# Optimization experiments

Measured on AMD Instinct MI355X. Metric: run time of the kernel, lower is better.

Reference implementation:

```python
import jax, jax.numpy as jnp
import numpy as np

B, N, D = 4, 300, 256
G, PIN, POUT = 4, 32, 128
CG = D // G
TOTAL = CG * CG + PIN * POUT
STRIDES = (8, 16, 32, 64)
SIZES = ((100, 160), (50, 80), (25, 40), (13, 20))
TAU = 2.0
MAP_STRIDE = 3.0  # log2(stride of level 0) = log2(8)


def setup_inputs():
    key = jax.random.key(0)
    ks = jax.random.split(key, 16)
    inp = {}
    for i, (h, w) in enumerate(SIZES):
        inp['feat%d' % i] = jax.random.normal(ks[i], (B, D, h, w), jnp.float32)
    inp['query_feat'] = jax.random.normal(ks[4], (B, N, D), jnp.float32)
    xy = jax.random.uniform(ks[5], (B, N, 2), jnp.float32) * jnp.array([1280.0, 800.0], jnp.float32)
    z = jax.random.uniform(ks[6], (B, N, 1), jnp.float32) * 2.0 + 4.0
    r = jax.random.normal(ks[7], (B, N, 1), jnp.float32) * 0.3
    inp['query_roi'] = jnp.concatenate([xy, z, r], axis=-1)
    inp['off_w'] = jax.random.normal(ks[8], (D, G * PIN * 3), jnp.float32) * 0.01
    bias = jnp.concatenate([jax.random.uniform(ks[9], (G, PIN, 2), jnp.float32, -0.5, 0.5),
                            jnp.full((G, PIN, 1), -1.0, jnp.float32)], axis=-1)
    inp['off_b'] = bias.reshape(-1)
    inp['pg_w'] = jax.random.normal(ks[10], (D, G * TOTAL), jnp.float32) * 0.02
    inp['pg_b'] = jnp.zeros((G * TOTAL,), jnp.float32)
    inp['op_w'] = jax.random.normal(ks[11], (G * POUT * CG, D), jnp.float32) * 0.01
    inp['op_b'] = jnp.zeros((D,), jnp.float32)
    inp['ln_g'] = jnp.ones((D,), jnp.float32)
    inp['ln_b'] = jnp.zeros((D,), jnp.float32)
    return inp


def _ln2(x, eps=1e-5):
    # F.layer_norm over last two dims, no affine
    mu = jnp.mean(x, axis=(-2, -1), keepdims=True)
    var = jnp.mean((x - mu) ** 2, axis=(-2, -1), keepdims=True)
    return (x - mu) * jax.lax.rsqrt(var + eps)


def _ln1(x, eps=1e-5):
    mu = jnp.mean(x, axis=-1, keepdims=True)
    var = jnp.mean((x - mu) ** 2, axis=-1, keepdims=True)
    return (x - mu) * jax.lax.rsqrt(var + eps)


def _bilinear(feat, px, py, w):
    # feat [B,D,H,W]; px,py,w [B,N,G,PIN] (pixel coords, grid_sample align_corners=False, zero pad)
    H, W = feat.shape[2], feat.shape[3]
    v = feat.reshape(B, G, CG, H * W).transpose(0, 1, 3, 2)  # [B,G,HW,CG]
    x0 = jnp.floor(px)
    y0 = jnp.floor(py)
    wx1 = px - x0
    wy1 = py - y0

    def corner(xf, yf, cw):
        xi = xf.astype(jnp.int32)
        yi = yf.astype(jnp.int32)
        valid = (xi >= 0) & (xi < W) & (yi >= 0) & (yi < H)
        idx = jnp.clip(yi, 0, H - 1) * W + jnp.clip(xi, 0, W - 1)       # [B,N,G,PIN]
        idx = idx.transpose(0, 2, 1, 3).reshape(B, G, N * PIN, 1)
        g = jnp.take_along_axis(v, idx, axis=2)                          # [B,G,N*PIN,CG]
        g = g.reshape(B, G, N, PIN, CG).transpose(0, 2, 1, 3, 4)
        return g * (cw * valid.astype(cw.dtype))[..., None]

    acc = (corner(x0, y0, (1 - wx1) * (1 - wy1)) + corner(x0 + 1, y0, wx1 * (1 - wy1)) +
           corner(x0, y0 + 1, (1 - wx1) * wy1) + corner(x0 + 1, y0 + 1, wx1 * wy1))
    return acc * w[..., None]


def _forward(feats, query_feat, query_roi, off_w, off_b, pg_w, pg_b, op_w, op_b, ln_g, ln_b):
    # make_sample_points
    offset = (query_feat @ off_w + off_b).reshape(B, N, G * PIN, 3)
    roi_cc = query_roi[..., :2]
    scale = 2.0 ** query_roi[..., 2:3]
    ratio = 2.0 ** jnp.concatenate([query_roi[..., 3:4] * -0.5, query_roi[..., 3:4] * 0.5], axis=-1)
    roi_wh = scale * ratio                                               # [B,N,2]
    sample_xy = roi_cc[:, :, None, :] + offset[..., :2] * roi_wh[:, :, None, :]  # [B,N,G*PIN,2]
    sample_z = query_roi[..., 2:3] + offset[..., 2]                      # [B,N,G*PIN]
    # level weights: softmax over levels of -(z-3-l)^2/tau
    lvl = jnp.arange(len(STRIDES), dtype=sample_z.dtype)
    lw = jax.nn.softmax(-((sample_z - MAP_STRIDE)[..., None] - lvl) ** 2 / TAU, axis=-1)
    sx = sample_xy[..., 0].reshape(B, N, G, PIN)
    sy = sample_xy[..., 1].reshape(B, N, G, PIN)
    sampled = jnp.zeros((B, N, G, PIN, CG), query_feat.dtype)
    for li, (feat, stride) in enumerate(zip(feats, STRIDES)):
        wl = lw[..., li].reshape(B, N, G, PIN)
        sampled = sampled + _bilinear(feat, sx / stride - 0.5, sy / stride - 0.5, wl)
    # AdaptiveMixing
    params = (query_feat @ pg_w + pg_b).reshape(B, N, G, TOTAL)
    M = params[..., :CG * CG].reshape(B, N, G, CG, CG)
    S = params[..., CG * CG:].reshape(B, N, G, POUT, PIN)
    h = jnp.einsum('bngpc,bngcd->bngpd', sampled, M)
    h = jax.nn.relu(_ln2(h))
    h = jnp.einsum('bngop,bngpd->bngod', S, h)
    h = jax.nn.relu(_ln2(h))
    h = query_feat + (h.reshape(B, N, G * POUT * CG) @ op_w + op_b)
    return _ln1(h) * ln_g + ln_b


def reference(feat0, feat1, feat2, feat3, query_feat, query_roi, off_w, off_b, pg_w, pg_b, op_w, op_b, ln_g, ln_b):
    return _forward([feat0, feat1, feat2, feat3], query_feat, query_roi,
                    off_w, off_b, pg_w, pg_b, op_w, op_b, ln_g, ln_b)
```

## Files before the change

### kernel.cpp

```cpp
#include <hip/hip_runtime.h>
#include <hip/hip_bf16.h>
#include <cstdint>

namespace {

constexpr int B = 4, N = 300, D = 256;
constexpr int G = 4, PIN = 32, POUT = 128;
constexpr int CG = D / G;
constexpr int TOTAL = CG * CG + PIN * POUT;
constexpr int BN_TOT = B * N;
constexpr int BN_PAD = 1216;
constexpr int GT = G * TOTAL;

typedef short s16x8 __attribute__((ext_vector_type(8)));
typedef float f32x4 __attribute__((ext_vector_type(4)));

__device__ __forceinline__ float bf2f(unsigned short u) {
  union { unsigned int i; float f; } x; x.i = ((unsigned int)u) << 16; return x.f;
}
__device__ __forceinline__ unsigned short f2bf(float f) {
  union { float f; unsigned int i; } x; x.f = f;
  unsigned int r = x.i + 0x7fffu + ((x.i >> 16) & 1u);
  return (unsigned short)(r >> 16);
}

__device__ __forceinline__ void breduce2(float& a, float& b, volatile float* red) {
  __syncthreads();
  #pragma unroll
  for (int off = 32; off; off >>= 1) {
    a += __shfl_down(a, off, 64);
    b += __shfl_down(b, off, 64);
  }
  int t = threadIdx.x;
  if ((t & 63) == 0) { red[t >> 6] = a; red[4 + (t >> 6)] = b; }
  __syncthreads();
  a = red[0] + red[1] + red[2] + red[3];
  b = red[4] + red[5] + red[6] + red[7];
}

__global__ __launch_bounds__(256) void k_transpose(
    const float* __restrict__ in, unsigned short* __restrict__ out, int R, int C,
    int mperm) {
  __shared__ unsigned short T[64][72];
  int c0 = blockIdx.x * 64;
  int r0 = blockIdx.y * 64;
  int t = threadIdx.x;
  #pragma unroll
  for (int i = 0; i < 4; ++i) {
    int u = t + i * 256;
    int rr = u >> 4, c4 = (u & 15) * 4;
    float4 v = *(const float4*)(in + (size_t)(r0 + rr) * C + c0 + c4);
    ushort4 w;
    w.x = f2bf(v.x); w.y = f2bf(v.y); w.z = f2bf(v.z); w.w = f2bf(v.w);
    *(ushort4*)&T[rr][c4] = w;
  }
  __syncthreads();
  #pragma unroll
  for (int i = 0; i < 2; ++i) {
    int u = t + i * 256;
    int c = u >> 3, rr8 = (u & 7) * 8;
    unsigned short tmp[8];
    #pragma unroll
    for (int j = 0; j < 8; ++j) tmp[j] = T[rr8 + j][c];
    int n = c0 + c;
    if (mperm) {
      int local = n & 8191;
      if (local < 4096) n = (n & ~8191) | ((local & 63) << 6) | (local >> 6);
    }
    *(uint4*)(out + (size_t)n * R + r0 + rr8) = *(const uint4*)tmp;
  }
}

__global__ __launch_bounds__(256) void k_featT(
    const float* __restrict__ in, unsigned short* __restrict__ out, int HW) {
  __shared__ unsigned short T[64][72];
  int hw0 = blockIdx.x * 64;
  int d0 = blockIdx.y * 64;
  int bb = blockIdx.z;
  int t = threadIdx.x;
  #pragma unroll
  for (int i = 0; i < 4; ++i) {
    int u = t + i * 256;
    int rr = u >> 4, c4 = (u & 15) * 4;
    if (hw0 + c4 + 3 < HW) {
      float4 v = *(const float4*)(in + ((size_t)(bb * D + d0 + rr)) * HW + hw0 + c4);
      ushort4 w;
      w.x = f2bf(v.x); w.y = f2bf(v.y); w.z = f2bf(v.z); w.w = f2bf(v.w);
      *(ushort4*)&T[rr][c4] = w;
    }
  }
  __syncthreads();
  #pragma unroll
  for (int i = 0; i < 2; ++i) {
    int u = t + i * 256;
    int p = u >> 3, dd8 = (u & 7) * 8;
    if (hw0 + p < HW) {
      unsigned short tmp[8];
      #pragma unroll
      for (int j = 0; j < 8; ++j) tmp[j] = T[dd8 + j][p];
      *(uint4*)(out + ((size_t)(bb * HW + hw0 + p)) * D + d0 + dd8) = *(const uint4*)tmp;
    }
  }
}

__global__ __launch_bounds__(256) void k_cvt_qf(
    const float* __restrict__ qf, unsigned short* __restrict__ qb) {
  int e = (blockIdx.x * 256 + threadIdx.x) * 4;
  int row = e >> 8;
  ushort4 w;
  if (row < BN_TOT) {
    float4 v = *(const float4*)(qf + e);
    w.x = f2bf(v.x); w.y = f2bf(v.y); w.z = f2bf(v.z); w.w = f2bf(v.w);
  } else {
    w.x = w.y = w.z = w.w = 0;
  }
  *(ushort4*)(qb + e) = w;
}

__global__ __launch_bounds__(384) void k_off(
    const float* __restrict__ qf, const float* __restrict__ offw,
    const float* __restrict__ offb, float* __restrict__ offsets) {
  int r0 = blockIdx.x * 16;
  int t = threadIdx.x;
  __shared__ float Q[16][256];
  for (int i = t; i < 16 * 256; i += 384)
    Q[i >> 8][i & 255] = qf[(size_t)(r0 + (i >> 8)) * 256 + (i & 255)];
  __syncthreads();
  float acc[16];
  float bias = offb[t];
  #pragma unroll
  for (int r = 0; r < 16; ++r) acc[r] = bias;
  for (int d = 0; d < 256; ++d) {
    float w = offw[(size_t)d * 384 + t];
    #pragma unroll
    for (int r = 0; r < 16; ++r) acc[r] += Q[r][d] * w;
  }
  #pragma unroll
  for (int r = 0; r < 16; ++r) offsets[(size_t)(r0 + r) * 384 + t] = acc[r];
}

__global__ __launch_bounds__(256) void k_gather(
    const float* __restrict__ roi, const float* __restrict__ offsets,
    const unsigned short* __restrict__ featT, unsigned short* __restrict__ sampled) {
  int bn = blockIdx.x;
  int bb = bn / N;
  int t = threadIdx.x;
  __shared__ int   widx[2048];
  __shared__ float wval[2048];

  const int Wl[4] = {160, 80, 40, 20};
  const int Hl[4] = {100, 50, 25, 13};
  const int loff[4] = {0, 16384000, 20480000, 21504000};
  const int HWl[4] = {16000, 4000, 1000, 260};
  const float sl[4] = {8.f, 16.f, 32.f, 64.f};

  float cx = roi[bn * 4 + 0], cy = roi[bn * 4 + 1];
  float z = roi[bn * 4 + 2], r = roi[bn * 4 + 3];
  float scale = exp2f(z);
  float rwx = scale * exp2f(-0.5f * r);
  float rhy = scale * exp2f(0.5f * r);

  #pragma unroll
  for (int task = t; task < 512; task += 256) {
    int j = task >> 2, l = task & 3;
    float ox = offsets[(size_t)bn * 384 + j * 3 + 0];
    float oy = offsets[(size_t)bn * 384 + j * 3 + 1];
    float oz = offsets[(size_t)bn * 384 + j * 3 + 2];
    float sx = cx + ox * rwx;
    float sy = cy + oy * rhy;
    float sz = z + oz;
    float lw[4];
    float m = -1e30f;
    #pragma unroll
    for (int ll = 0; ll < 4; ++ll) {
      float dlt = sz - 3.0f - (float)ll;
      lw[ll] = -dlt * dlt * 0.5f;
      m = fmaxf(m, lw[ll]);
    }
    float s = 0.f;
    #pragma unroll
    for (int ll = 0; ll < 4; ++ll) { lw[ll] = expf(lw[ll] - m); s += lw[ll]; }
    float wl_ = lw[l] / s;

    int W = Wl[l], H = Hl[l];
    float px = sx / sl[l] - 0.5f;
    float py = sy / sl[l] - 0.5f;
    float x0f = floorf(px), y0f = floorf(py);
    int x0 = (int)x0f, y0 = (int)y0f;
    float fx = px - x0f, fy = py - y0f;
    int base = loff[l] + bb * HWl[l] * 256;
    #pragma unroll
    for (int k = 0; k < 4; ++k) {
      int xi = x0 + (k & 1), yi = y0 + (k >> 1);
      bool valid = (xi >= 0) & (xi < W) & (yi >= 0) & (yi < H);
      int xc = min(max(xi, 0), W - 1), yc = min(max(yi, 0), H - 1);
      float wgt = ((k & 1) ? fx : 1.f - fx) * ((k >> 1) ? fy : 1.f - fy) * wl_;
      widx[j * 16 + l * 4 + k] = base + (yc * W + xc) * 256;
      wval[j * 16 + l * 4 + k] = valid ? wgt : 0.f;
    }
  }
  __syncthreads();

  int wave = t >> 6, lane = t & 63;
  int half = lane >> 5, ln = lane & 31;
  const unsigned short* fb = featT + wave * 64 + ln * 2;
  #pragma unroll 2
  for (int it = 0; it < 16; ++it) {
    int p = it * 2 + half;
    int j = wave * 32 + p;
    int ix[16]; float w[16]; unsigned int u[16];
    #pragma unroll
    for (int k = 0; k < 16; ++k) { ix[k] = widx[j * 16 + k]; w[k] = wval[j * 16 + k]; }
    #pragma unroll
    for (int k = 0; k < 16; ++k) u[k] = *(const unsigned int*)(fb + ix[k]);
    float a0 = 0.f, a1 = 0.f;
    #pragma unroll
    for (int k = 0; k < 16; ++k) {
      a0 += w[k] * bf2f((unsigned short)(u[k] & 0xffffu));
      a1 += w[k] * bf2f((unsigned short)(u[k] >> 16));
    }
    unsigned int packed = (unsigned int)f2bf(a0) | ((unsigned int)f2bf(a1) << 16);
    *(unsigned int*)(sampled + (((size_t)bn * G + wave) * PIN + p) * CG + ln * 2) = packed;
  }
}

__global__ __launch_bounds__(256) void k_pgemm(
    const unsigned short* __restrict__ A, const unsigned short* __restrict__ Bt,
    const float* __restrict__ pgb, unsigned short* __restrict__ params) {
  __shared__ unsigned short As[64][72];
  __shared__ unsigned short Bs[128][72];
  int col0 = blockIdx.x * 128;
  int row0 = blockIdx.y * 64;
  int t = threadIdx.x;
  int wave = t >> 6, lane = t & 63, lr = lane & 15, q = lane >> 4;
  f32x4 acc[4][2] = {};
  for (int k0 = 0; k0 < D; k0 += 64) {
    #pragma unroll
    for (int i = 0; i < 2; ++i) {
      int u = t + i * 256;
      int r = u >> 3, kk = (u & 7) * 8;
      *(uint4*)&As[r][kk] = *(const uint4*)(A + (size_t)(row0 + r) * D + k0 + kk);
    }
    #pragma unroll
    for (int i = 0; i < 4; ++i) {
      int u = t + i * 256;
      int n = u >> 3, kk = (u & 7) * 8;
      *(uint4*)&Bs[n][kk] = *(const uint4*)(Bt + (size_t)(col0 + n) * D + k0 + kk);
    }
    __syncthreads();
    #pragma unroll
    for (int ks = 0; ks < 64; ks += 32) {
      s16x8 af[4], bf[2];
      #pragma unroll
      for (int mi = 0; mi < 4; ++mi)
        af[mi] = *(const s16x8*)&As[mi * 16 + lr][ks + q * 8];
      #pragma unroll
      for (int ni = 0; ni < 2; ++ni)
        bf[ni] = *(const s16x8*)&Bs[wave * 32 + ni * 16 + lr][ks + q * 8];
      #pragma unroll
      for (int mi = 0; mi < 4; ++mi)
        #pragma unroll
        for (int ni = 0; ni < 2; ++ni)
          acc[mi][ni] = __builtin_amdgcn_mfma_f32_16x16x32_bf16(af[mi], bf[ni], acc[mi][ni], 0, 0, 0);
    }
    __syncthreads();
  }
  #pragma unroll
  for (int ni = 0; ni < 2; ++ni) {
    int c = col0 + wave * 32 + ni * 16 + lr;
    int local = c & 8191;
    int cb = (local < 4096) ? ((c & ~8191) | ((local & 63) << 6) | (local >> 6)) : c;
    float bias = pgb[cb];
    #pragma unroll
    for (int mi = 0; mi < 4; ++mi) {
      #pragma unroll
      for (int rg = 0; rg < 4; ++rg) {
        int rr = row0 + mi * 16 + q * 4 + rg;
        if (rr < BN_TOT) params[(size_t)rr * GT + c] = f2bf(acc[mi][ni][rg] + bias);
      }
    }
  }
}

__global__ __launch_bounds__(256) void k_mixing(
    const unsigned short* __restrict__ sampled,
    const unsigned short* __restrict__ params,
    unsigned short* __restrict__ h2out) {
  int blk = blockIdx.x;
  int g = blk & 3, bn = blk >> 2;
  const unsigned short* P = params + (size_t)bn * GT + (size_t)g * TOTAL;
  const unsigned short* Sp = sampled + (((size_t)bn * G + g) * PIN) * CG;
  __shared__ unsigned short Ht[64][40];
  __shared__ float red[8];
  int t = threadIdx.x;
  int w = t >> 6, lane = t & 63, lr = lane & 15, q = lane >> 4;

  f32x4 acc1[2] = {};
  #pragma unroll
  for (int ks = 0; ks < 2; ++ks) {
    s16x8 b = *(const s16x8*)(P + (w * 16 + lr) * 64 + ks * 32 + q * 8);
    #pragma unroll
    for (int mt = 0; mt < 2; ++mt) {
      s16x8 a = *(const s16x8*)(Sp + (mt * 16 + lr) * 64 + ks * 32 + q * 8);
      acc1[mt] = __builtin_amdgcn_mfma_f32_16x16x32_bf16(a, b, acc1[mt], 0, 0, 0);
    }
  }
  float s1 = 0.f, ss1 = 0.f;
  #pragma unroll
  for (int mt = 0; mt < 2; ++mt)
    #pragma unroll
    for (int rg = 0; rg < 4; ++rg) { float v = acc1[mt][rg]; s1 += v; ss1 += v * v; }
  breduce2(s1, ss1, red);
  {
    float mu = s1 * (1.f / 2048.f);
    float var = ss1 * (1.f / 2048.f) - mu * mu;
    float rs = rsqrtf(var + 1e-5f);
    #pragma unroll
    for (int mt = 0; mt < 2; ++mt) {
      unsigned short pk[4];
      #pragma unroll
      for (int rg = 0; rg < 4; ++rg) {
        float v = (acc1[mt][rg] - mu) * rs;
        pk[rg] = f2bf(v > 0.f ? v : 0.f);
      }
      *(uint2*)&Ht[w * 16 + lr][mt * 16 + q * 4] = *(const uint2*)pk;
    }
  }
  __syncthreads();

  f32x4 acc2[2][4] = {};
  #pragma unroll
  for (int mt = 0; mt < 2; ++mt) {
    int o = w * 32 + mt * 16 + lr;
    s16x8 a = *(const s16x8*)(P + 4096 + o * 32 + q * 8);
    #pragma unroll
    for (int nt = 0; nt < 4; ++nt) {
      s16x8 b = *(const s16x8*)&Ht[nt * 16 + lr][q * 8];
      acc2[mt][nt] = __builtin_amdgcn_mfma_f32_16x16x32_bf16(a, b, acc2[mt][nt], 0, 0, 0);
    }
  }
  float s2 = 0.f, ss2 = 0.f;
  #pragma unroll
  for (int mt = 0; mt < 2; ++mt)
    #pragma unroll
    for (int nt = 0; nt < 4; ++nt)
      #pragma unroll
      for (int rg = 0; rg < 4; ++rg) { float v = acc2[mt][nt][rg]; s2 += v; ss2 += v * v; }
  breduce2(s2, ss2, red);
  {
    float mu = s2 * (1.f / 8192.f);
    float var = ss2 * (1.f / 8192.f) - mu * mu;
    float rs = rsqrtf(var + 1e-5f);
    unsigned short* dst = h2out + (size_t)bn * GT + (size_t)g * TOTAL;
    #pragma unroll
    for (int mt = 0; mt < 2; ++mt) {
      #pragma unroll
      for (int nt = 0; nt < 4; ++nt) {
        int d = nt * 16 + lr;
        #pragma unroll
        for (int rg = 0; rg < 4; ++rg) {
          int o = w * 32 + mt * 16 + q * 4 + rg;
          float v = (acc2[mt][nt][rg] - mu) * rs;
          dst[o * 64 + d] = f2bf(v > 0.f ? v : 0.f);
        }
      }
    }
  }
}

constexpr int KSPLIT = 32, KCH = GT / KSPLIT;
__global__ __launch_bounds__(256) void k_ogemm(
    const unsigned short* __restrict__ A, const unsigned short* __restrict__ Bt,
    float* __restrict__ parts) {
  __shared__ unsigned short As[64][72];
  __shared__ unsigned short Bs[256][72];
  int row0 = blockIdx.x * 64;
  int z = blockIdx.y;
  int kbase = z * KCH;
  int t = threadIdx.x;
  int wave = t >> 6, lane = t & 63, lr = lane & 15, q = lane >> 4;
  f32x4 acc[4][4] = {};
  for (int k0 = 0; k0 < KCH; k0 += 64) {
    #pragma unroll
    for (int i = 0; i < 2; ++i) {
      int u = t + i * 256;
      int r = u >> 3, kk = (u & 7) * 8;
      *(uint4*)&As[r][kk] = *(const uint4*)(A + (size_t)(row0 + r) * GT + kbase + k0 + kk);
    }
    #pragma unroll
    for (int i = 0; i < 8; ++i) {
      int u = t + i * 256;
      int n = u >> 3, kk = (u & 7) * 8;
      *(uint4*)&Bs[n][kk] = *(const uint4*)(Bt + (size_t)n * GT + kbase + k0 + kk);
    }
    __syncthreads();
    #pragma unroll
    for (int ks = 0; ks < 64; ks += 32) {
      s16x8 af[4], bf[4];
      #pragma unroll
      for (int mi = 0; mi < 4; ++mi)
        af[mi] = *(const s16x8*)&As[mi * 16 + lr][ks + q * 8];
      #pragma unroll
      for (int ni = 0; ni < 4; ++ni)
        bf[ni] = *(const s16x8*)&Bs[wave * 64 + ni * 16 + lr][ks + q * 8];
      #pragma unroll
      for (int mi = 0; mi < 4; ++mi)
        #pragma unroll
        for (int ni = 0; ni < 4; ++ni)
          acc[mi][ni] = __builtin_amdgcn_mfma_f32_16x16x32_bf16(af[mi], bf[ni], acc[mi][ni], 0, 0, 0);
    }
    __syncthreads();
  }
  #pragma unroll
  for (int mi = 0; mi < 4; ++mi) {
    #pragma unroll
    for (int ni = 0; ni < 4; ++ni) {
      int c = wave * 64 + ni * 16 + lr;
      #pragma unroll
      for (int rg = 0; rg < 4; ++rg) {
        int rr = row0 + mi * 16 + q * 4 + rg;
        if (rr < BN_TOT)
          parts[((size_t)z * BN_PAD + rr) * D + c] = acc[mi][ni][rg];
      }
    }
  }
}

__global__ __launch_bounds__(256) void k_final(
    const float* __restrict__ qf, const float* __restrict__ opb,
    const float* __restrict__ parts, const float* __restrict__ lng,
    const float* __restrict__ lnb, float* __restrict__ out) {
  int bn = blockIdx.x;
  int d = threadIdx.x;
  float v = qf[(size_t)bn * D + d] + opb[d];
  #pragma unroll
  for (int s = 0; s < KSPLIT; ++s) v += parts[((size_t)s * BN_PAD + bn) * D + d];
  __shared__ float red[8];
  float a = v, b2 = v * v;
  breduce2(a, b2, red);
  float mu = a * (1.f / D);
  float var = b2 * (1.f / D) - mu * mu;
  float rs = rsqrtf(var + 1e-5f);
  out[(size_t)bn * D + d] = (v - mu) * rs * lng[d] + lnb[d];
}

}

extern "C" void kernel_launch(void* const* d_in, const int* in_sizes, int n_in,
                              void* d_out, int out_size, void* d_ws, size_t ws_size,
                              hipStream_t stream) {
  const float* f0 = (const float*)d_in[0];
  const float* f1 = (const float*)d_in[1];
  const float* f2 = (const float*)d_in[2];
  const float* f3 = (const float*)d_in[3];
  const float* qf = (const float*)d_in[4];
  const float* roi = (const float*)d_in[5];
  const float* off_w = (const float*)d_in[6];
  const float* off_b = (const float*)d_in[7];
  const float* pg_w = (const float*)d_in[8];
  const float* pg_b = (const float*)d_in[9];
  const float* op_w = (const float*)d_in[10];
  const float* op_b = (const float*)d_in[11];
  const float* ln_g = (const float*)d_in[12];
  const float* ln_b = (const float*)d_in[13];
  float* out = (float*)d_out;

  char* ws = (char*)d_ws;
  unsigned short* sampled = (unsigned short*)ws;
  unsigned short* h2      = (unsigned short*)(ws + 19660800ULL);
  unsigned short* featT   = h2;
  unsigned short* params  = (unsigned short*)(ws + 19660800ULL + 79691776ULL);
  float*          parts   = (float*)(ws + 19660800ULL + 79691776ULL);
  unsigned short* wT      = (unsigned short*)(ws + 19660800ULL + 2 * 79691776ULL);
  unsigned short* qfb     = (unsigned short*)(ws + 19660800ULL + 2 * 79691776ULL + 16777216ULL);
  float*          offsets = (float*)(ws + 19660800ULL + 2 * 79691776ULL + 16777216ULL + 622592ULL);

  k_featT<<<dim3(250, 4, B), 256, 0, stream>>>(f0, featT + 0,        16000);
  k_featT<<<dim3( 63, 4, B), 256, 0, stream>>>(f1, featT + 16384000, 4000);
  k_featT<<<dim3( 16, 4, B), 256, 0, stream>>>(f2, featT + 20480000, 1000);
  k_featT<<<dim3(  5, 4, B), 256, 0, stream>>>(f3, featT + 21504000, 260);
  k_off<<<BN_TOT / 16, 384, 0, stream>>>(qf, off_w, off_b, offsets);
  k_transpose<<<dim3(GT / 64, D / 64), 256, 0, stream>>>(pg_w, wT, D, GT, 1);
  k_cvt_qf<<<BN_PAD * D / 1024, 256, 0, stream>>>(qf, qfb);
  k_gather<<<BN_TOT, 256, 0, stream>>>(roi, offsets, featT, sampled);
  k_pgemm<<<dim3(GT / 128, BN_PAD / 64), 256, 0, stream>>>(qfb, wT, pg_b, params);
  k_mixing<<<BN_TOT * G, 256, 0, stream>>>(sampled, params, h2);
  k_transpose<<<dim3(D / 64, GT / 64), 256, 0, stream>>>(op_w, wT, GT, D, 0);
  k_ogemm<<<dim3(BN_PAD / 64, KSPLIT), 256, 0, stream>>>(h2, wT, parts);
  k_final<<<BN_TOT, 256, 0, stream>>>(qf, op_b, parts, ln_g, ln_b, out);
}
```

Measured before the change: 421.1 us.

## Use direct global-to-LDS loads with XOR swizzle in both GEMMs; widen pgemm tile

Both GEMM kernels now load their A and B tiles straight into LDS with global_load_lds, skipping the register round-trip. The LDS layout drops row padding and instead uses an XOR swizzle on the 16-byte chunks, which keeps fragment reads free of bank conflicts. The pgemm block tile grows from 128 to 256 columns, so each A tile is reused across more output columns and the grid is half as large. The price is more accumulator registers per thread and fewer blocks in flight for pgemm.

```diff
diff --git a/kernel.cpp b/kernel.cpp
--- a/kernel.cpp
+++ b/kernel.cpp
@@ -22,6 +22,12 @@
   union { float f; unsigned int i; } x; x.f = f;
   unsigned int r = x.i + 0x7fffu + ((x.i >> 16) & 1u);
   return (unsigned short)(r >> 16);
+}
+
+__device__ __forceinline__ void gld_lds16(const void* g, void* l) {
+  __builtin_amdgcn_global_load_lds(
+      (const __attribute__((address_space(1))) unsigned int*)g,
+      (__attribute__((address_space(3))) unsigned int*)l, 16, 0, 0);
 }
 
 __device__ __forceinline__ void breduce2(float& a, float& b, volatile float* red) {
@@ -227,47 +233,52 @@
 __global__ __launch_bounds__(256) void k_pgemm(
     const unsigned short* __restrict__ A, const unsigned short* __restrict__ Bt,
     const float* __restrict__ pgb, unsigned short* __restrict__ params) {
-  __shared__ unsigned short As[64][72];
-  __shared__ unsigned short Bs[128][72];
-  int col0 = blockIdx.x * 128;
+  __shared__ __attribute__((aligned(16))) unsigned short As[64 * 64];
+  __shared__ __attribute__((aligned(16))) unsigned short Bs[256 * 64];
+  int col0 = blockIdx.x * 256;
   int row0 = blockIdx.y * 64;
   int t = threadIdx.x;
-  int wave = t >> 6, lane = t & 63, lr = lane & 15, q = lane >> 4;
-  f32x4 acc[4][2] = {};
+  int w = t >> 6, lane = t & 63, lr = lane & 15, q = lane >> 4;
+  int srow = lane >> 3;
+  int sc16 = (lane & 7) ^ srow;
+  f32x4 acc[4][4] = {};
   for (int k0 = 0; k0 < D; k0 += 64) {
     #pragma unroll
     for (int i = 0; i < 2; ++i) {
-      int u = t + i * 256;
-      int r = u >> 3, kk = (u & 7) * 8;
-      *(uint4*)&As[r][kk] = *(const uint4*)(A + (size_t)(row0 + r) * D + k0 + kk);
-    }
-    #pragma unroll
-    for (int i = 0; i < 4; ++i) {
-      int u = t + i * 256;
-      int n = u >> 3, kk = (u & 7) * 8;
-      *(uint4*)&Bs[n][kk] = *(const uint4*)(Bt + (size_t)(col0 + n) * D + k0 + kk);
+      int n = (w * 2 + i) * 8 + srow;
+      gld_lds16(A + (size_t)(row0 + n) * D + k0 + sc16 * 8, As + (w * 2 + i) * 512);
+    }
+    #pragma unroll
+    for (int i = 0; i < 8; ++i) {
+      int n = (w * 8 + i) * 8 + srow;
+      gld_lds16(Bt + (size_t)(col0 + n) * D + k0 + sc16 * 8, Bs + (w * 8 + i) * 512);
     }
     __syncthreads();
     #pragma unroll
-    for (int ks = 0; ks < 64; ks += 32) {
-      s16x8 af[4], bf[2];
-      #pragma unroll
-      for (int mi = 0; mi < 4; ++mi)
-        af[mi] = *(const s16x8*)&As[mi * 16 + lr][ks + q * 8];
-      #pragma unroll
-      for (int ni = 0; ni < 2; ++ni)
-        bf[ni] = *(const s16x8*)&Bs[wave * 32 + ni * 16 + lr][ks + q * 8];
+    for (int ks = 0; ks < 2; ++ks) {
+      int c16 = ks * 4 + q;
+      s16x8 af[4], bf[4];
+      #pragma unroll
+      for (int mi = 0; mi < 4; ++mi) {
+        int rrow = mi * 16 + lr;
+        af[mi] = *(const s16x8*)(As + rrow * 64 + ((c16 ^ (rrow & 7)) * 8));
+      }
+      #pragma unroll
+      for (int ni = 0; ni < 4; ++ni) {
+        int brow = w * 64 + ni * 16 + lr;
+        bf[ni] = *(const s16x8*)(Bs + brow * 64 + ((c16 ^ (brow & 7)) * 8));
+      }
       #pragma unroll
       for (int mi = 0; mi < 4; ++mi)
         #pragma unroll
-        for (int ni = 0; ni < 2; ++ni)
+        for (int ni = 0; ni < 4; ++ni)
           acc[mi][ni] = __builtin_amdgcn_mfma_f32_16x16x32_bf16(af[mi], bf[ni], acc[mi][ni], 0, 0, 0);
     }
     __syncthreads();
   }
   #pragma unroll
-  for (int ni = 0; ni < 2; ++ni) {
-    int c = col0 + wave * 32 + ni * 16 + lr;
+  for (int ni = 0; ni < 4; ++ni) {
+    int c = col0 + w * 64 + ni * 16 + lr;
     int local = c & 8191;
     int cb = (local < 4096) ? ((c & ~8191) | ((local & 63) << 6) | (local >> 6)) : c;
     float bias = pgb[cb];
@@ -372,37 +383,42 @@
 __global__ __launch_bounds__(256) void k_ogemm(
     const unsigned short* __restrict__ A, const unsigned short* __restrict__ Bt,
     float* __restrict__ parts) {
-  __shared__ unsigned short As[64][72];
-  __shared__ unsigned short Bs[256][72];
+  __shared__ __attribute__((aligned(16))) unsigned short As[64 * 64];
+  __shared__ __attribute__((aligned(16))) unsigned short Bs[256 * 64];
   int row0 = blockIdx.x * 64;
   int z = blockIdx.y;
   int kbase = z * KCH;
   int t = threadIdx.x;
-  int wave = t >> 6, lane = t & 63, lr = lane & 15, q = lane >> 4;
+  int w = t >> 6, lane = t & 63, lr = lane & 15, q = lane >> 4;
+  int srow = lane >> 3;
+  int sc16 = (lane & 7) ^ srow;
   f32x4 acc[4][4] = {};
   for (int k0 = 0; k0 < KCH; k0 += 64) {
     #pragma unroll
     for (int i = 0; i < 2; ++i) {
-      int u = t + i * 256;
-      int r = u >> 3, kk = (u & 7) * 8;
-      *(uint4*)&As[r][kk] = *(const uint4*)(A + (size_t)(row0 + r) * GT + kbase + k0 + kk);
+      int n = (w * 2 + i) * 8 + srow;
+      gld_lds16(A + (size_t)(row0 + n) * GT + kbase + k0 + sc16 * 8, As + (w * 2 + i) * 512);
     }
     #pragma unroll
     for (int i = 0; i < 8; ++i) {
-      int u = t + i * 256;
-      int n = u >> 3, kk = (u & 7) * 8;
-      *(uint4*)&Bs[n][kk] = *(const uint4*)(Bt + (size_t)n * GT + kbase + k0 + kk);
+      int n = (w * 8 + i) * 8 + srow;
+      gld_lds16(Bt + (size_t)n * GT + kbase + k0 + sc16 * 8, Bs + (w * 8 + i) * 512);
     }
     __syncthreads();
     #pragma unroll
-    for (int ks = 0; ks < 64; ks += 32) {
+    for (int ks = 0; ks < 2; ++ks) {
+      int c16 = ks * 4 + q;
       s16x8 af[4], bf[4];
       #pragma unroll
-      for (int mi = 0; mi < 4; ++mi)
-        af[mi] = *(const s16x8*)&As[mi * 16 + lr][ks + q * 8];
-      #pragma unroll
-      for (int ni = 0; ni < 4; ++ni)
-        bf[ni] = *(const s16x8*)&Bs[wave * 64 + ni * 16 + lr][ks + q * 8];
+      for (int mi = 0; mi < 4; ++mi) {
+        int rrow = mi * 16 + lr;
+        af[mi] = *(const s16x8*)(As + rrow * 64 + ((c16 ^ (rrow & 7)) * 8));
+      }
+      #pragma unroll
+      for (int ni = 0; ni < 4; ++ni) {
+        int brow = w * 64 + ni * 16 + lr;
+        bf[ni] = *(const s16x8*)(Bs + brow * 64 + ((c16 ^ (brow & 7)) * 8));
+      }
       #pragma unroll
       for (int mi = 0; mi < 4; ++mi)
         #pragma unroll
@@ -415,7 +431,7 @@
   for (int mi = 0; mi < 4; ++mi) {
     #pragma unroll
     for (int ni = 0; ni < 4; ++ni) {
-      int c = wave * 64 + ni * 16 + lr;
+      int c = w * 64 + ni * 16 + lr;
       #pragma unroll
       for (int rg = 0; rg < 4; ++rg) {
         int rr = row0 + mi * 16 + q * 4 + rg;
@@ -483,7 +499,7 @@
   k_transpose<<<dim3(GT / 64, D / 64), 256, 0, stream>>>(pg_w, wT, D, GT, 1);
   k_cvt_qf<<<BN_PAD * D / 1024, 256, 0, stream>>>(qf, qfb);
   k_gather<<<BN_TOT, 256, 0, stream>>>(roi, offsets, featT, sampled);
-  k_pgemm<<<dim3(GT / 128, BN_PAD / 64), 256, 0, stream>>>(qfb, wT, pg_b, params);
+  k_pgemm<<<dim3(GT / 256, BN_PAD / 64), 256, 0, stream>>>(qfb, wT, pg_b, params);
   k_mixing<<<BN_TOT * G, 256, 0, stream>>>(sampled, params, h2);
   k_transpose<<<dim3(D / 64, GT / 64), 256, 0, stream>>>(op_w, wT, GT, D, 0);
   k_ogemm<<<dim3(BN_PAD / 64, KSPLIT), 256, 0, stream>>>(h2, wT, parts);
```

Result: slower. 436.3 us (+3.6%).
